# Optimization experiments

Measured on AMD Instinct MI355X. Metric: run time of the kernel, lower is better.

The kernel has to match this reference:

```python
import jax, jax.numpy as jnp
import numpy as np

N_TOK, EMBED, N_CLS, BATCH, N_HEAD = 32768, 512, 16, 8, 8
D_HEAD = EMBED // N_HEAD


def setup_inputs() -> dict:
    key0 = jax.random.key(0)
    ks = jax.random.split(key0, 12)
    s = 1.0 / np.sqrt(EMBED)
    query = jax.random.normal(ks[0], (N_TOK, EMBED), dtype=jnp.float32)
    key_f = jax.random.normal(ks[1], (N_CLS, BATCH, EMBED), dtype=jnp.float32)
    val_f = jax.random.normal(ks[2], (N_CLS, BATCH, EMBED), dtype=jnp.float32)
    batch_idx = jnp.sort(jax.random.randint(ks[3], (N_TOK,), 0, BATCH)).astype(jnp.int32)
    Wq = jax.random.normal(ks[4], (EMBED, EMBED), dtype=jnp.float32) * s
    bq = jnp.zeros((EMBED,), dtype=jnp.float32)
    Wk = jax.random.normal(ks[5], (EMBED, EMBED), dtype=jnp.float32) * s  # Conv1d(k=1) kernel squeezed
    bk = jnp.zeros((EMBED,), dtype=jnp.float32)
    Wv = jax.random.normal(ks[6], (EMBED, EMBED), dtype=jnp.float32) * s
    bv = jnp.zeros((EMBED,), dtype=jnp.float32)
    Wo = jax.random.normal(ks[7], (EMBED, EMBED), dtype=jnp.float32) * s
    bo = jnp.zeros((EMBED,), dtype=jnp.float32)
    return {"query": query, "key": key_f, "value": val_f, "batch_idx": batch_idx,
            "batch_size": BATCH, "Wq": Wq, "bq": bq, "Wk": Wk, "bk": bk,
            "Wv": Wv, "bv": bv, "Wo": Wo, "bo": bo}


def reference(query, key, value, batch_idx, batch_size, Wq, bq, Wk, bk, Wv, bv, Wo, bo):
    n_tok, embed = query.shape
    L, B, _ = key.shape
    H, D = N_HEAD, EMBED // N_HEAD
    scale = D ** -0.5  # matmul_norm
    # projections (Conv1d with kernel_size=1 == pointwise linear over E)
    q = (query @ Wq.T + bq).reshape(n_tok, H, D)                           # [N,H,D]
    k = (jnp.einsum('lbe,fe->blf', key, Wk) + bk)                          # [B,L,E]
    k = k.transpose(0, 2, 1).reshape(B, H, D, L)                           # [B,H,D,L]
    v = (jnp.einsum('lbe,fe->blf', value, Wv) + bv)                        # [B,L,E]
    v = v.transpose(0, 2, 1).reshape(B, H, D, L).transpose(0, 1, 3, 2)     # [B,H,L,D]
    # scores against every batch's prototypes, then pick each token's batch
    scores_all = jnp.einsum('nhd,bhdl->nbhl', q, k) * scale                # [N,B,H,L]
    sel = batch_idx.astype(jnp.int32)[:, None, None, None]
    scores = jnp.take_along_axis(scores_all, sel, axis=1).squeeze(1)       # [N,H,L]
    p = jax.nn.softmax(scores, axis=-1)
    ctx_all = jnp.einsum('nhl,bhld->nbhd', p, v)                           # [N,B,H,D]
    ctx = jnp.take_along_axis(ctx_all, sel, axis=1).squeeze(1)             # [N,H,D]
    return ctx.reshape(n_tok, embed) @ Wo.T + bo
```

## Files before the change

### kernel.cpp

```cpp
#include <hip/hip_runtime.h>

typedef unsigned short u16;
typedef __attribute__((ext_vector_type(8))) short short8;
typedef __attribute__((ext_vector_type(4))) unsigned short u16x4;
typedef __attribute__((ext_vector_type(4))) float f32x4;

#define N_TOKENS 32768
#define EMBED 512
#define NCLS 16
#define NBATCH 8
#define NHEAD 8
#define DHEAD 64

__device__ __forceinline__ u16 f2bf(float f) {
  unsigned u = __float_as_uint(f);
  u += 0x7fffu + ((u >> 16) & 1u);
  return (u16)(u >> 16);
}

__device__ __forceinline__ void async16(const u16* g, u16* l) {
  __builtin_amdgcn_global_load_lds(
      (__attribute__((address_space(1))) const unsigned int*)(const void*)g,
      (__attribute__((address_space(3))) unsigned int*)(void*)l,
      16, 0, 0);
}

__global__ __launch_bounds__(256) void kvproj_kernel(
    const float* __restrict__ key, const float* __restrict__ val,
    const float* __restrict__ Wk, const float* __restrict__ bk,
    const float* __restrict__ Wv, const float* __restrict__ bv,
    float* __restrict__ kproj, float* __restrict__ vproj) {
  const int blk = blockIdx.x;
  const bool isV = blk & 1;
  const int b = (blk >> 1) & 7;
  const int l = (blk >> 4) & 15;
  const int fg = blk >> 8;
  const int wave = threadIdx.x >> 6;
  const int lane = threadIdx.x & 63;
  const int fbase = fg * 64 + wave * 16;
  const float* x = (isV ? val : key) + ((size_t)l * NBATCH + b) * EMBED;
  const float* W = isV ? Wv : Wk;
  const float* bias = isV ? bv : bk;

  float4 x0 = *(const float4*)(x + lane * 8);
  float4 x1 = *(const float4*)(x + lane * 8 + 4);

#pragma unroll
  for (int grp = 0; grp < 4; grp++) {
    float acc[4];
#pragma unroll
    for (int j = 0; j < 4; j++) {
      const float* w = W + (size_t)(fbase + grp * 4 + j) * EMBED + lane * 8;
      float4 w0 = *(const float4*)w;
      float4 w1 = *(const float4*)(w + 4);
      acc[j] = x0.x * w0.x + x0.y * w0.y + x0.z * w0.z + x0.w * w0.w +
               x1.x * w1.x + x1.y * w1.y + x1.z * w1.z + x1.w * w1.w;
    }
#pragma unroll
    for (int j = 0; j < 4; j++) {
      acc[j] += __shfl_xor(acc[j], 1);
      acc[j] += __shfl_xor(acc[j], 2);
      acc[j] += __shfl_xor(acc[j], 4);
      acc[j] += __shfl_xor(acc[j], 8);
      acc[j] += __shfl_xor(acc[j], 16);
      acc[j] += __shfl_xor(acc[j], 32);
    }
#pragma unroll
    for (int j = 0; j < 4; j++) {
      if (lane == j) {
        const int f = fbase + grp * 4 + j;
        float v = acc[j] + bias[f];
        if (!isV) {
          kproj[((size_t)(b * EMBED + f)) * NCLS + l] = v;
        } else {
          vproj[(size_t)b * 8192 + (size_t)(f >> 6) * 1024 + l * 64 + (f & 63)] = v;
        }
      }
    }
  }
}

__global__ __launch_bounds__(256) void build_all(
    const float* __restrict__ kproj, const float* __restrict__ vproj,
    const float* __restrict__ Wq, const float* __restrict__ bq,
    const float* __restrict__ Wo,
    u16* __restrict__ Kqb, u16* __restrict__ WoVb, float* __restrict__ sb) {
  const int blk = blockIdx.x;
  if (blk < 2048) {
    int t = blk * 256 + threadIdx.x;
    int e = t & 511;
    int hl = (t >> 9) & 127;
    int b = t >> 16;
    int h = hl >> 4, l = hl & 15;
    const float* kp = kproj + (size_t)b * 8192 + h * 1024 + l;
    const float* wq = Wq + (size_t)(h * 64) * 512 + e;
    float acc = 0.f;
#pragma unroll 16
    for (int d = 0; d < 64; d++) acc += kp[d * 16] * wq[d * 512];
    Kqb[t] = f2bf(acc);
  } else if (blk < 3072) {
    const int wave = threadIdx.x >> 6;
    const int lane = threadIdx.x & 63;
    const int wgid = (blk - 2048) * 4 + wave;
    const int b = wgid >> 9, f = wgid & 511;
    const int l = lane >> 2, c = lane & 3;
    const float* vp = vproj + (size_t)b * 8192 + l * 64 + c * 16;
    const float* wo = Wo + (size_t)f * 512 + c * 16;
#pragma unroll 2
    for (int h = 0; h < 8; h++) {
      const float* v = vp + h * 1024;
      const float* w = wo + h * 64;
      float4 v0 = *(const float4*)v,       w0 = *(const float4*)w;
      float4 v1 = *(const float4*)(v + 4), w1 = *(const float4*)(w + 4);
      float4 v2 = *(const float4*)(v + 8), w2 = *(const float4*)(w + 8);
      float4 v3 = *(const float4*)(v + 12), w3 = *(const float4*)(w + 12);
      float acc = v0.x * w0.x + v0.y * w0.y + v0.z * w0.z + v0.w * w0.w +
                  v1.x * w1.x + v1.y * w1.y + v1.z * w1.z + v1.w * w1.w +
                  v2.x * w2.x + v2.y * w2.y + v2.z * w2.z + v2.w * w2.w +
                  v3.x * w3.x + v3.y * w3.y + v3.z * w3.z + v3.w * w3.w;
      acc += __shfl_xor(acc, 1);
      acc += __shfl_xor(acc, 2);
      if (c == 0) WoVb[(size_t)b * 65536 + (size_t)f * 128 + h * 16 + l] = f2bf(acc);
    }
  } else {
    int t = (blk - 3072) * 256 + threadIdx.x;
    int hl = t & 127, b = t >> 7;
    int h = hl >> 4, l = hl & 15;
    const float* kp = kproj + (size_t)b * 8192 + h * 1024 + l;
    const float* q = bq + h * 64;
    float acc = 0.f;
#pragma unroll
    for (int d = 0; d < 64; d++) acc += q[d] * kp[d * 16];
    sb[t] = acc;
  }
}

__global__ __launch_bounds__(256) void fused_attn(
    const float* __restrict__ query, const u16* __restrict__ Kqb,
    const u16* __restrict__ WoVb, const float* __restrict__ sb,
    const float* __restrict__ bo, const int* __restrict__ bidx,
    float* __restrict__ out) {
  __shared__ __align__(16) u16 Bs[2][128 * 32];
  __shared__ __align__(16) u16 Ps[64 * 128];
  const int tid = threadIdx.x;
  const int lane = tid & 63;
  const int wave = tid >> 6;
  const int quad = lane >> 4;
  const int l16 = lane & 15;
  const int tileId = blockIdx.x & 511;
  const int slot = blockIdx.x >> 9;
  const int m0 = tileId * 64;
  const int bFirst = bidx[m0];
  const int bLast = bidx[m0 + 63];
  if (slot == 1 && bFirst == bLast) return;
  const int b0 = (slot == 0) ? bFirst : bFirst + 1;
  const int b1 = (slot == 0) ? bFirst : bLast;

  const int r0 = tid >> 2, r1 = r0 + 64;
  const int lg0 = (tid & 3) ^ ((r0 >> 1) & 3);
  const int lg1 = (tid & 3) ^ ((r1 >> 1) & 3);
  const size_t boff0 = (size_t)r0 * 512 + lg0 * 8;
  const size_t boff1 = (size_t)r1 * 512 + lg1 * 8;

  const float* pA = query + (size_t)(m0 + wave * 16 + l16) * 512 + quad * 8;

  for (int bb = b0; bb <= b1; bb++) {
    const u16* Bq = Kqb + (size_t)bb * 65536;

    async16(Bq + boff0, &Bs[0][tid * 8]);
    async16(Bq + boff1, &Bs[0][tid * 8 + 2048]);
    float4 a0c = *(const float4*)(pA);
    float4 a1c = *(const float4*)(pA + 4);

    f32x4 acc1[8];
#pragma unroll
    for (int j = 0; j < 8; j++) acc1[j] = (f32x4){0.f, 0.f, 0.f, 0.f};

    for (int t = 0; t < 16; t++) {
      __syncthreads();
      const int cur = t & 1;
      if (t < 15) {
        const int ko = (t + 1) * 32;
        async16(Bq + boff0 + ko, &Bs[cur ^ 1][tid * 8]);
        async16(Bq + boff1 + ko, &Bs[cur ^ 1][tid * 8 + 2048]);
      }
      float4 a0 = a0c, a1 = a1c;
      if (t < 15) {
        a0c = *(const float4*)(pA + (t + 1) * 32);
        a1c = *(const float4*)(pA + (t + 1) * 32 + 4);
      }
      short8 af;
      af[0] = (short)f2bf(a0.x); af[1] = (short)f2bf(a0.y);
      af[2] = (short)f2bf(a0.z); af[3] = (short)f2bf(a0.w);
      af[4] = (short)f2bf(a1.x); af[5] = (short)f2bf(a1.y);
      af[6] = (short)f2bf(a1.z); af[7] = (short)f2bf(a1.w);
      __builtin_amdgcn_s_setprio(1);
#pragma unroll
      for (int ni = 0; ni < 8; ni++) {
        const int rw = ni * 16 + l16;
        short8 bfr = *(const short8*)&Bs[cur][rw * 32 + ((quad ^ ((rw >> 1) & 3)) << 3)];
        acc1[ni] = __builtin_amdgcn_mfma_f32_16x16x32_bf16(af, bfr, acc1[ni], 0, 0, 0);
      }
      __builtin_amdgcn_s_setprio(0);
    }

    float sbv[8];
#pragma unroll
    for (int ni = 0; ni < 8; ni++) sbv[ni] = sb[bb * 128 + ni * 16 + l16];
#pragma unroll
    for (int r = 0; r < 4; r++) {
      const int row = wave * 16 + quad * 4 + r;
#pragma unroll
      for (int ni = 0; ni < 8; ni++) {
        float v = acc1[ni][r] + sbv[ni];
        float ev = __expf(v * 0.125f);
        float s = ev;
        s += __shfl_xor(s, 1);
        s += __shfl_xor(s, 2);
        s += __shfl_xor(s, 4);
        s += __shfl_xor(s, 8);
        const int col = ni * 16 + l16;
        Ps[row * 128 + (((col >> 3) ^ (row & 7)) << 3) + (col & 7)] = f2bf(ev / s);
      }
    }
    __syncthreads();

    const u16* Wv = WoVb + (size_t)bb * 65536;
#pragma unroll
    for (int h2 = 0; h2 < 2; h2++) {
#pragma unroll
      for (int nh = 0; nh < 2; nh++) {
        const int f0 = wave * 128 + h2 * 64 + nh * 32;
        f32x4 acc2[4][2];
#pragma unroll
        for (int i = 0; i < 4; i++)
#pragma unroll
          for (int j = 0; j < 2; j++) acc2[i][j] = (f32x4){0.f, 0.f, 0.f, 0.f};
#pragma unroll
        for (int kk = 0; kk < 4; kk++) {
          short8 paf[4], bf2[2];
#pragma unroll
          for (int mi = 0; mi < 4; mi++) {
            const int row = mi * 16 + l16;
            paf[mi] = *(const short8*)&Ps[row * 128 + (((kk * 4 + quad) ^ (row & 7)) << 3)];
          }
#pragma unroll
          for (int nj = 0; nj < 2; nj++) {
            const int fr = f0 + nj * 16 + l16;
            bf2[nj] = *(const short8*)(Wv + (size_t)fr * 128 + kk * 32 + quad * 8);
          }
          __builtin_amdgcn_s_setprio(1);
#pragma unroll
          for (int mi = 0; mi < 4; mi++)
#pragma unroll
            for (int nj = 0; nj < 2; nj++)
              acc2[mi][nj] = __builtin_amdgcn_mfma_f32_16x16x32_bf16(paf[mi], bf2[nj], acc2[mi][nj], 0, 0, 0);
          __builtin_amdgcn_s_setprio(0);
        }
        float bov[2];
#pragma unroll
        for (int nj = 0; nj < 2; nj++) bov[nj] = bo[f0 + nj * 16 + l16];
#pragma unroll
        for (int mi = 0; mi < 4; mi++)
#pragma unroll
          for (int r = 0; r < 4; r++) {
            const int rb = bidx[m0 + mi * 16 + quad * 4 + r];
            if (rb == bb) {
              const size_t row = m0 + mi * 16 + quad * 4 + r;
#pragma unroll
              for (int nj = 0; nj < 2; nj++)
                out[row * 512 + f0 + nj * 16 + l16] = acc2[mi][nj][r] + bov[nj];
            }
          }
      }
    }
    __syncthreads();
  }
}

extern "C" void kernel_launch(void* const* d_in, const int* in_sizes, int n_in,
                              void* d_out, int out_size, void* d_ws, size_t ws_size,
                              hipStream_t stream) {
  const float* query = (const float*)d_in[0];
  const float* keyt = (const float*)d_in[1];
  const float* valt = (const float*)d_in[2];
  const int* bidx = (const int*)d_in[3];
  const float* Wq = (const float*)d_in[5];
  const float* bq = (const float*)d_in[6];
  const float* Wk = (const float*)d_in[7];
  const float* bk = (const float*)d_in[8];
  const float* Wv = (const float*)d_in[9];
  const float* bv = (const float*)d_in[10];
  const float* Wo = (const float*)d_in[11];
  const float* bo = (const float*)d_in[12];
  float* out = (float*)d_out;

  unsigned char* w = (unsigned char*)d_ws;
  float* kproj = (float*)(w + 41943040ull);
  float* vproj = (float*)(w + 42205184ull);
  u16* Kqb = (u16*)(w + 42467328ull);
  u16* WoVb = (u16*)(w + 43515904ull);
  float* sb = (float*)(w + 44564480ull);

  kvproj_kernel<<<2048, 256, 0, stream>>>(keyt, valt, Wk, bk, Wv, bv, kproj, vproj);

  build_all<<<3076, 256, 0, stream>>>(kproj, vproj, Wq, bq, Wo, Kqb, WoVb, sb);

  fused_attn<<<N_TOKENS / 64 * 2, 256, 0, stream>>>(query, Kqb, WoVb, sb, bo, bidx, out);
}
```

Before: 236.1 us.

## Halve token tile to 32 rows and split score GEMM across 2x2 waves

The fused attention kernel now processes 32 tokens per block instead of 64, doubling the grid. The four waves are arranged 2x2 over rows and score columns in the first GEMM, and the output GEMM is reshaped to 2x4 MFMA tiles per wave. This is meant to raise the number of active blocks per CU and shorten per-block work, at the cost of reloading the Kq and WoV tiles twice as often per token. It also adds a per-head max subtraction to the softmax, which costs extra shuffles but improves numerical stability.

New measurement: 222.7 us. -5.7%, faster.

```diff
diff --git a/kernel.cpp b/kernel.cpp
--- a/kernel.cpp
+++ b/kernel.cpp
@@ -141,17 +141,17 @@
     const float* __restrict__ bo, const int* __restrict__ bidx,
     float* __restrict__ out) {
   __shared__ __align__(16) u16 Bs[2][128 * 32];
-  __shared__ __align__(16) u16 Ps[64 * 128];
+  __shared__ __align__(16) u16 Ps[32 * 128];
   const int tid = threadIdx.x;
   const int lane = tid & 63;
   const int wave = tid >> 6;
   const int quad = lane >> 4;
   const int l16 = lane & 15;
-  const int tileId = blockIdx.x & 511;
-  const int slot = blockIdx.x >> 9;
-  const int m0 = tileId * 64;
+  const int tileId = blockIdx.x & 1023;
+  const int slot = blockIdx.x >> 10;
+  const int m0 = tileId * 32;
   const int bFirst = bidx[m0];
-  const int bLast = bidx[m0 + 63];
+  const int bLast = bidx[m0 + 31];
   if (slot == 1 && bFirst == bLast) return;
   const int b0 = (slot == 0) ? bFirst : bFirst + 1;
   const int b1 = (slot == 0) ? bFirst : bLast;
@@ -162,7 +162,10 @@
   const size_t boff0 = (size_t)r0 * 512 + lg0 * 8;
   const size_t boff1 = (size_t)r1 * 512 + lg1 * 8;
 
-  const float* pA = query + (size_t)(m0 + wave * 16 + l16) * 512 + quad * 8;
+  const int wr = (wave & 1) * 16;
+  const int wcb = (wave >> 1) * 64;
+
+  const float* pA = query + (size_t)(m0 + wr + l16) * 512 + quad * 8;
 
   for (int bb = b0; bb <= b1; bb++) {
     const u16* Bq = Kqb + (size_t)bb * 65536;
@@ -172,9 +175,9 @@
     float4 a0c = *(const float4*)(pA);
     float4 a1c = *(const float4*)(pA + 4);
 
-    f32x4 acc1[8];
-#pragma unroll
-    for (int j = 0; j < 8; j++) acc1[j] = (f32x4){0.f, 0.f, 0.f, 0.f};
+    f32x4 acc1[4];
+#pragma unroll
+    for (int j = 0; j < 4; j++) acc1[j] = (f32x4){0.f, 0.f, 0.f, 0.f};
 
     for (int t = 0; t < 16; t++) {
       __syncthreads();
@@ -196,30 +199,35 @@
       af[6] = (short)f2bf(a1.z); af[7] = (short)f2bf(a1.w);
       __builtin_amdgcn_s_setprio(1);
 #pragma unroll
-      for (int ni = 0; ni < 8; ni++) {
-        const int rw = ni * 16 + l16;
+      for (int ni = 0; ni < 4; ni++) {
+        const int rw = wcb + ni * 16 + l16;
         short8 bfr = *(const short8*)&Bs[cur][rw * 32 + ((quad ^ ((rw >> 1) & 3)) << 3)];
         acc1[ni] = __builtin_amdgcn_mfma_f32_16x16x32_bf16(af, bfr, acc1[ni], 0, 0, 0);
       }
       __builtin_amdgcn_s_setprio(0);
     }
 
-    float sbv[8];
-#pragma unroll
-    for (int ni = 0; ni < 8; ni++) sbv[ni] = sb[bb * 128 + ni * 16 + l16];
+    float sbv[4];
+#pragma unroll
+    for (int ni = 0; ni < 4; ni++) sbv[ni] = sb[bb * 128 + wcb + ni * 16 + l16];
 #pragma unroll
     for (int r = 0; r < 4; r++) {
-      const int row = wave * 16 + quad * 4 + r;
-#pragma unroll
-      for (int ni = 0; ni < 8; ni++) {
+      const int row = wr + quad * 4 + r;
+#pragma unroll
+      for (int ni = 0; ni < 4; ni++) {
         float v = acc1[ni][r] + sbv[ni];
-        float ev = __expf(v * 0.125f);
+        float mx = v;
+        mx = fmaxf(mx, __shfl_xor(mx, 1));
+        mx = fmaxf(mx, __shfl_xor(mx, 2));
+        mx = fmaxf(mx, __shfl_xor(mx, 4));
+        mx = fmaxf(mx, __shfl_xor(mx, 8));
+        float ev = __expf((v - mx) * 0.125f);
         float s = ev;
         s += __shfl_xor(s, 1);
         s += __shfl_xor(s, 2);
         s += __shfl_xor(s, 4);
         s += __shfl_xor(s, 8);
-        const int col = ni * 16 + l16;
+        const int col = wcb + ni * 16 + l16;
         Ps[row * 128 + (((col >> 3) ^ (row & 7)) << 3) + (col & 7)] = f2bf(ev / s);
       }
     }
@@ -228,51 +236,48 @@
     const u16* Wv = WoVb + (size_t)bb * 65536;
 #pragma unroll
     for (int h2 = 0; h2 < 2; h2++) {
-#pragma unroll
-      for (int nh = 0; nh < 2; nh++) {
-        const int f0 = wave * 128 + h2 * 64 + nh * 32;
-        f32x4 acc2[4][2];
-#pragma unroll
-        for (int i = 0; i < 4; i++)
-#pragma unroll
-          for (int j = 0; j < 2; j++) acc2[i][j] = (f32x4){0.f, 0.f, 0.f, 0.f};
-#pragma unroll
-        for (int kk = 0; kk < 4; kk++) {
-          short8 paf[4], bf2[2];
-#pragma unroll
-          for (int mi = 0; mi < 4; mi++) {
-            const int row = mi * 16 + l16;
-            paf[mi] = *(const short8*)&Ps[row * 128 + (((kk * 4 + quad) ^ (row & 7)) << 3)];
+      const int f0 = wave * 128 + h2 * 64;
+      f32x4 acc2[2][4];
+#pragma unroll
+      for (int i = 0; i < 2; i++)
+#pragma unroll
+        for (int j = 0; j < 4; j++) acc2[i][j] = (f32x4){0.f, 0.f, 0.f, 0.f};
+#pragma unroll
+      for (int kk = 0; kk < 4; kk++) {
+        short8 paf[2], bf2[4];
+#pragma unroll
+        for (int mi = 0; mi < 2; mi++) {
+          const int row = mi * 16 + l16;
+          paf[mi] = *(const short8*)&Ps[row * 128 + (((kk * 4 + quad) ^ (row & 7)) << 3)];
+        }
+#pragma unroll
+        for (int ni = 0; ni < 4; ni++) {
+          const int fr = f0 + ni * 16 + l16;
+          bf2[ni] = *(const short8*)(Wv + (size_t)fr * 128 + kk * 32 + quad * 8);
+        }
+        __builtin_amdgcn_s_setprio(1);
+#pragma unroll
+        for (int mi = 0; mi < 2; mi++)
+#pragma unroll
+          for (int ni = 0; ni < 4; ni++)
+            acc2[mi][ni] = __builtin_amdgcn_mfma_f32_16x16x32_bf16(paf[mi], bf2[ni], acc2[mi][ni], 0, 0, 0);
+        __builtin_amdgcn_s_setprio(0);
+      }
+      float bov[4];
+#pragma unroll
+      for (int ni = 0; ni < 4; ni++) bov[ni] = bo[f0 + ni * 16 + l16];
+#pragma unroll
+      for (int mi = 0; mi < 2; mi++)
+#pragma unroll
+        for (int r = 0; r < 4; r++) {
+          const int rb = bidx[m0 + mi * 16 + quad * 4 + r];
+          if (rb == bb) {
+            const size_t row = m0 + mi * 16 + quad * 4 + r;
+#pragma unroll
+            for (int ni = 0; ni < 4; ni++)
+              out[row * 512 + f0 + ni * 16 + l16] = acc2[mi][ni][r] + bov[ni];
           }
-#pragma unroll
-          for (int nj = 0; nj < 2; nj++) {
-            const int fr = f0 + nj * 16 + l16;
-            bf2[nj] = *(const short8*)(Wv + (size_t)fr * 128 + kk * 32 + quad * 8);
-          }
-          __builtin_amdgcn_s_setprio(1);
-#pragma unroll
-          for (int mi = 0; mi < 4; mi++)
-#pragma unroll
-            for (int nj = 0; nj < 2; nj++)
-              acc2[mi][nj] = __builtin_amdgcn_mfma_f32_16x16x32_bf16(paf[mi], bf2[nj], acc2[mi][nj], 0, 0, 0);
-          __builtin_amdgcn_s_setprio(0);
         }
-        float bov[2];
-#pragma unroll
-        for (int nj = 0; nj < 2; nj++) bov[nj] = bo[f0 + nj * 16 + l16];
-#pragma unroll
-        for (int mi = 0; mi < 4; mi++)
-#pragma unroll
-          for (int r = 0; r < 4; r++) {
-            const int rb = bidx[m0 + mi * 16 + quad * 4 + r];
-            if (rb == bb) {
-              const size_t row = m0 + mi * 16 + quad * 4 + r;
-#pragma unroll
-              for (int nj = 0; nj < 2; nj++)
-                out[row * 512 + f0 + nj * 16 + l16] = acc2[mi][nj][r] + bov[nj];
-            }
-          }
-      }
     }
     __syncthreads();
   }
@@ -306,5 +311,5 @@
 
   build_all<<<3076, 256, 0, stream>>>(kproj, vproj, Wq, bq, Wo, Kqb, WoVb, sb);
 
-  fused_attn<<<N_TOKENS / 64 * 2, 256, 0, stream>>>(query, Kqb, WoVb, sb, bo, bidx, out);
-}
+  fused_attn<<<N_TOKENS / 32 * 2, 256, 0, stream>>>(query, Kqb, WoVb, sb, bo, bidx, out);
+}
```

## Preload query fragments into registers, widen output tile, add max-subtracted softmax

Applied to the files above, without the earlier changes.

Converts the whole query row slice to bf16 MFMA fragments once before the batch loop and fully unrolls the k-loop. This avoids reloading and reconverting query for each batch a tile spans. The output GEMM now computes a 64-column block per pass with a 4x4 accumulator instead of two 32-column passes, which reuses the P fragments more. Softmax now subtracts the row max for numerical safety, which adds shuffles. The extra accumulators and the 16 preloaded fragments raise register pressure and can reduce occupancy.

New measurement: 228.1 us. 3.4% less time.

```diff
diff --git a/kernel.cpp b/kernel.cpp
--- a/kernel.cpp
+++ b/kernel.cpp
@@ -163,19 +163,30 @@
   const size_t boff1 = (size_t)r1 * 512 + lg1 * 8;
 
   const float* pA = query + (size_t)(m0 + wave * 16 + l16) * 512 + quad * 8;
+  short8 aReg[16];
+#pragma unroll
+  for (int t = 0; t < 16; t++) {
+    float4 a0 = *(const float4*)(pA + t * 32);
+    float4 a1 = *(const float4*)(pA + t * 32 + 4);
+    short8 v;
+    v[0] = (short)f2bf(a0.x); v[1] = (short)f2bf(a0.y);
+    v[2] = (short)f2bf(a0.z); v[3] = (short)f2bf(a0.w);
+    v[4] = (short)f2bf(a1.x); v[5] = (short)f2bf(a1.y);
+    v[6] = (short)f2bf(a1.z); v[7] = (short)f2bf(a1.w);
+    aReg[t] = v;
+  }
 
   for (int bb = b0; bb <= b1; bb++) {
     const u16* Bq = Kqb + (size_t)bb * 65536;
 
     async16(Bq + boff0, &Bs[0][tid * 8]);
     async16(Bq + boff1, &Bs[0][tid * 8 + 2048]);
-    float4 a0c = *(const float4*)(pA);
-    float4 a1c = *(const float4*)(pA + 4);
 
     f32x4 acc1[8];
 #pragma unroll
     for (int j = 0; j < 8; j++) acc1[j] = (f32x4){0.f, 0.f, 0.f, 0.f};
 
+#pragma unroll
     for (int t = 0; t < 16; t++) {
       __syncthreads();
       const int cur = t & 1;
@@ -184,22 +195,12 @@
         async16(Bq + boff0 + ko, &Bs[cur ^ 1][tid * 8]);
         async16(Bq + boff1 + ko, &Bs[cur ^ 1][tid * 8 + 2048]);
       }
-      float4 a0 = a0c, a1 = a1c;
-      if (t < 15) {
-        a0c = *(const float4*)(pA + (t + 1) * 32);
-        a1c = *(const float4*)(pA + (t + 1) * 32 + 4);
-      }
-      short8 af;
-      af[0] = (short)f2bf(a0.x); af[1] = (short)f2bf(a0.y);
-      af[2] = (short)f2bf(a0.z); af[3] = (short)f2bf(a0.w);
-      af[4] = (short)f2bf(a1.x); af[5] = (short)f2bf(a1.y);
-      af[6] = (short)f2bf(a1.z); af[7] = (short)f2bf(a1.w);
       __builtin_amdgcn_s_setprio(1);
 #pragma unroll
       for (int ni = 0; ni < 8; ni++) {
         const int rw = ni * 16 + l16;
         short8 bfr = *(const short8*)&Bs[cur][rw * 32 + ((quad ^ ((rw >> 1) & 3)) << 3)];
-        acc1[ni] = __builtin_amdgcn_mfma_f32_16x16x32_bf16(af, bfr, acc1[ni], 0, 0, 0);
+        acc1[ni] = __builtin_amdgcn_mfma_f32_16x16x32_bf16(aReg[t], bfr, acc1[ni], 0, 0, 0);
       }
       __builtin_amdgcn_s_setprio(0);
     }
@@ -213,7 +214,12 @@
 #pragma unroll
       for (int ni = 0; ni < 8; ni++) {
         float v = acc1[ni][r] + sbv[ni];
-        float ev = __expf(v * 0.125f);
+        float mx = v;
+        mx = fmaxf(mx, __shfl_xor(mx, 1));
+        mx = fmaxf(mx, __shfl_xor(mx, 2));
+        mx = fmaxf(mx, __shfl_xor(mx, 4));
+        mx = fmaxf(mx, __shfl_xor(mx, 8));
+        float ev = __expf((v - mx) * 0.125f);
         float s = ev;
         s += __shfl_xor(s, 1);
         s += __shfl_xor(s, 2);
@@ -228,51 +234,48 @@
     const u16* Wv = WoVb + (size_t)bb * 65536;
 #pragma unroll
     for (int h2 = 0; h2 < 2; h2++) {
-#pragma unroll
-      for (int nh = 0; nh < 2; nh++) {
-        const int f0 = wave * 128 + h2 * 64 + nh * 32;
-        f32x4 acc2[4][2];
-#pragma unroll
-        for (int i = 0; i < 4; i++)
-#pragma unroll
-          for (int j = 0; j < 2; j++) acc2[i][j] = (f32x4){0.f, 0.f, 0.f, 0.f};
-#pragma unroll
-        for (int kk = 0; kk < 4; kk++) {
-          short8 paf[4], bf2[2];
-#pragma unroll
-          for (int mi = 0; mi < 4; mi++) {
-            const int row = mi * 16 + l16;
-            paf[mi] = *(const short8*)&Ps[row * 128 + (((kk * 4 + quad) ^ (row & 7)) << 3)];
+      const int f0 = wave * 128 + h2 * 64;
+      f32x4 acc2[4][4];
+#pragma unroll
+      for (int i = 0; i < 4; i++)
+#pragma unroll
+        for (int j = 0; j < 4; j++) acc2[i][j] = (f32x4){0.f, 0.f, 0.f, 0.f};
+#pragma unroll
+      for (int kk = 0; kk < 4; kk++) {
+        short8 paf[4], bf2[4];
+#pragma unroll
+        for (int mi = 0; mi < 4; mi++) {
+          const int row = mi * 16 + l16;
+          paf[mi] = *(const short8*)&Ps[row * 128 + (((kk * 4 + quad) ^ (row & 7)) << 3)];
+        }
+#pragma unroll
+        for (int ni = 0; ni < 4; ni++) {
+          const int fr = f0 + ni * 16 + l16;
+          bf2[ni] = *(const short8*)(Wv + (size_t)fr * 128 + kk * 32 + quad * 8);
+        }
+        __builtin_amdgcn_s_setprio(1);
+#pragma unroll
+        for (int mi = 0; mi < 4; mi++)
+#pragma unroll
+          for (int ni = 0; ni < 4; ni++)
+            acc2[mi][ni] = __builtin_amdgcn_mfma_f32_16x16x32_bf16(paf[mi], bf2[ni], acc2[mi][ni], 0, 0, 0);
+        __builtin_amdgcn_s_setprio(0);
+      }
+      float bov[4];
+#pragma unroll
+      for (int ni = 0; ni < 4; ni++) bov[ni] = bo[f0 + ni * 16 + l16];
+#pragma unroll
+      for (int mi = 0; mi < 4; mi++)
+#pragma unroll
+        for (int r = 0; r < 4; r++) {
+          const int rb = bidx[m0 + mi * 16 + quad * 4 + r];
+          if (rb == bb) {
+            const size_t row = m0 + mi * 16 + quad * 4 + r;
+#pragma unroll
+            for (int ni = 0; ni < 4; ni++)
+              out[row * 512 + f0 + ni * 16 + l16] = acc2[mi][ni][r] + bov[ni];
           }
-#pragma unroll
-          for (int nj = 0; nj < 2; nj++) {
-            const int fr = f0 + nj * 16 + l16;
-            bf2[nj] = *(const short8*)(Wv + (size_t)fr * 128 + kk * 32 + quad * 8);
-          }
-          __builtin_amdgcn_s_setprio(1);
-#pragma unroll
-          for (int mi = 0; mi < 4; mi++)
-#pragma unroll
-            for (int nj = 0; nj < 2; nj++)
-              acc2[mi][nj] = __builtin_amdgcn_mfma_f32_16x16x32_bf16(paf[mi], bf2[nj], acc2[mi][nj], 0, 0, 0);
-          __builtin_amdgcn_s_setprio(0);
         }
-        float bov[2];
-#pragma unroll
-        for (int nj = 0; nj < 2; nj++) bov[nj] = bo[f0 + nj * 16 + l16];
-#pragma unroll
-        for (int mi = 0; mi < 4; mi++)
-#pragma unroll
-          for (int r = 0; r < 4; r++) {
-            const int rb = bidx[m0 + mi * 16 + quad * 4 + r];
-            if (rb == bb) {
-              const size_t row = m0 + mi * 16 + quad * 4 + r;
-#pragma unroll
-              for (int nj = 0; nj < 2; nj++)
-                out[row * 512 + f0 + nj * 16 + l16] = acc2[mi][nj][r] + bov[nj];
-            }
-          }
-      }
     }
     __syncthreads();
   }
```
